# Kernel optimization log

Hardware: AMD Instinct MI355X
Metric: run time of the kernel (lower is better)

## Reference

```python
import jax, jax.numpy as jnp
import numpy as np

DIM = 256
NUM_HEADS = 4
HEAD_DIM = DIM // NUM_HEADS
SCALE = HEAD_DIM ** -0.5


def setup_inputs() -> dict:
    key = jax.random.key(0)
    ks = jax.random.split(key, 11)
    B, Nq, Nkv = 4, 2048, 2048
    inp = {
        "query_feat": jax.random.normal(ks[0], (B, Nq, DIM), dtype=jnp.float32),
        "key_value_feat": jax.random.normal(ks[1], (B, Nkv, DIM), dtype=jnp.float32),
        "reliability_kv": jax.random.uniform(ks[2], (B, Nkv), dtype=jnp.float32),
        "Wq": jax.random.normal(ks[3], (DIM, DIM), dtype=jnp.float32) * (DIM ** -0.5),
        "bq": jnp.zeros((DIM,), jnp.float32),
        "Wk": jax.random.normal(ks[4], (DIM, DIM), dtype=jnp.float32) * (DIM ** -0.5),
        "bk": jnp.zeros((DIM,), jnp.float32),
        "Wv": jax.random.normal(ks[5], (DIM, DIM), dtype=jnp.float32) * (DIM ** -0.5),
        "bv": jnp.zeros((DIM,), jnp.float32),
        "Wo": jax.random.normal(ks[6], (DIM, DIM), dtype=jnp.float32) * (DIM ** -0.5),
        "bo": jnp.zeros((DIM,), jnp.float32),
    }
    return inp


def _heads(x):
    B, N, C = x.shape
    return x.reshape(B, N, NUM_HEADS, HEAD_DIM).transpose(0, 2, 1, 3)  # [B,H,N,hd]


def reference(query_feat, key_value_feat, reliability_kv, Wq, bq, Wk, bk, Wv, bv, Wo, bo):
    B, Nq, _ = query_feat.shape
    q = _heads(query_feat @ Wq + bq)          # [B,H,Nq,hd]
    k = _heads(key_value_feat @ Wk + bk)      # [B,H,Nkv,hd]
    v = _heads(key_value_feat @ Wv + bv)
    # gate K/V by reliability (broadcast over heads and head_dim)
    rk = reliability_kv[:, None, :, None]     # [B,1,Nkv,1]
    k = k * rk
    v = v * rk
    attn = jnp.einsum("bhqd,bhkd->bhqk", q, k) * SCALE
    log_r = jnp.log(jnp.clip(reliability_kv, 1e-6))[:, None, None, :]  # [B,1,1,Nkv]
    attn = jax.nn.softmax(attn + log_r, axis=-1)  # [B,H,Nq,Nkv]
    out = jnp.einsum("bhqk,bhkd->bhqd", attn, v)
    out = out.transpose(0, 2, 1, 3).reshape(B, Nq, DIM)
    out = out @ Wo + bo
    attn_mean = attn.mean(axis=1)  # [B,Nq,Nkv]
    return out, attn_mean
```

## Files before the change

### kernel.cpp

```cpp
#include <hip/hip_runtime.h>


typedef __attribute__((ext_vector_type(8))) _Float16 half8;
typedef __attribute__((ext_vector_type(4))) _Float16 half4;
typedef __attribute__((ext_vector_type(2))) __fp16 fp16x2;
typedef __attribute__((ext_vector_type(4))) float f32x4;

#define MFMAH32(A, B, C) __builtin_amdgcn_mfma_f32_16x16x32_f16((A), (B), (C), 0, 0, 0)
#define MFMAH16(A, B, C) __builtin_amdgcn_mfma_f32_16x16x16f16((A), (B), (C), 0, 0, 0)

__device__ __forceinline__ unsigned short f2h(float f) {
    union { _Float16 h; unsigned short u; } c; c.h = (_Float16)f; return c.u;
}
__device__ __forceinline__ float h2f(unsigned short u) {
    union { unsigned short u; _Float16 h; } c; c.u = u; return (float)c.h;
}
__device__ __forceinline__ half8 ldh8(const unsigned short* p) {
    return *reinterpret_cast<const half8*>(p);
}
__device__ __forceinline__ half4 ldh4(const unsigned short* p) {
    return *reinterpret_cast<const half4*>(p);
}
__device__ __forceinline__ half4 pk4(float a, float b, float c, float d) {
    union { fp16x2 h2[2]; half4 h4; } u;
    u.h2[0] = __builtin_amdgcn_cvt_pkrtz(a, b);
    u.h2[1] = __builtin_amdgcn_cvt_pkrtz(c, d);
    return u.h4;
}
__device__ __forceinline__ void gld16(const unsigned short* g, unsigned short* l) {
    __builtin_amdgcn_global_load_lds(
        (const __attribute__((address_space(1))) unsigned int*)g,
        (__attribute__((address_space(3))) unsigned int*)l, 16, 0, 0);
}

__global__ void wsplit_kernel(const float* __restrict__ Wq, const float* __restrict__ Wk,
                              const float* __restrict__ Wv, const float* __restrict__ Wo,
                              unsigned short* __restrict__ WT) {
    int e = blockIdx.x * 256 + threadIdx.x;
    int m = e >> 16;
    int idx = e & 65535;
    int k = idx >> 8, n = idx & 255;
    const float* W = (m == 0) ? Wq : (m == 1) ? Wk : (m == 2) ? Wv : Wo;
    WT[m * 65536 + n * 256 + k] = f2h(W[idx]);
}

#define STAGE_W(dst_, src_, kt_) do {                                               \
    _Pragma("unroll")                                                               \
    for (int j_ = 0; j_ < 4; ++j_) {                                                \
        int s_ = w * 4 + j_;                                                        \
        int rowl_ = 8 * s_ + (l >> 3);                                              \
        int so_ = rowl_ * 256 + (kt_) * 64 + (((l & 7) ^ (rowl_ & 7)) << 3);        \
        gld16(&(src_)[so_], &(dst_)[s_ * 512]);                                     \
    }                                                                               \
} while (0)

#define GEMM_TILE(buf_, kt_) do {                                                   \
    _Pragma("unroll")                                                               \
    for (int ksl_ = 0; ksl_ < 2; ++ksl_) {                                          \
        _Pragma("unroll")                                                           \
        for (int n_ = 0; n_ < 16; ++n_) {                                           \
            int r_ = n_ * 16 + l15;                                                 \
            int idx_ = r_ * 64 + ((((ksl_)*4 + lg) ^ (r_ & 7)) << 3);               \
            half8 b_ = ldh8(&(buf_)[idx_]);                                         \
            acc[n_] = MFMAH32(ah[(kt_) * 2 + ksl_], b_, acc[n_]);                   \
        }                                                                           \
    }                                                                               \
} while (0)

__global__ __launch_bounds__(512, 1) void proj3_kernel(
    const float* __restrict__ query, const float* __restrict__ kv,
    const float* __restrict__ rel, const unsigned short* __restrict__ WT,
    const float* __restrict__ bq, const float* __restrict__ bk, const float* __restrict__ bv,
    unsigned short* __restrict__ Qh, unsigned short* __restrict__ Kh,
    unsigned short* __restrict__ Vtmp) {
    const int job = blockIdx.y;
    const float* X = (job == 0) ? query : kv;
    const unsigned short* wg = WT + job * 65536;
    const float* bias = (job == 0) ? bq : (job == 1) ? bk : bv;
    const float* rs = (job == 0) ? nullptr : rel;
    unsigned short* oh = (job == 0) ? Qh : (job == 1) ? Kh : Vtmp;

    __shared__ __align__(16) unsigned short wlds[2][256 * 64];

    const int w = threadIdx.x >> 6, l = threadIdx.x & 63;
    const int l15 = l & 15, lg = l >> 4;
    const int arow = blockIdx.x * 128 + w * 16 + l15;

    half8 ah[8];
#pragma unroll
    for (int ks = 0; ks < 8; ++ks) {
        const float* p = &X[arow * 256 + ks * 32 + lg * 8];
        float4 f0 = *reinterpret_cast<const float4*>(p);
        float4 f1 = *reinterpret_cast<const float4*>(p + 4);
        half8 t;
        t[0] = (_Float16)f0.x; t[1] = (_Float16)f0.y; t[2] = (_Float16)f0.z; t[3] = (_Float16)f0.w;
        t[4] = (_Float16)f1.x; t[5] = (_Float16)f1.y; t[6] = (_Float16)f1.z; t[7] = (_Float16)f1.w;
        ah[ks] = t;
    }
    f32x4 acc[16];
#pragma unroll
    for (int n = 0; n < 16; ++n) acc[n] = (f32x4){0.f, 0.f, 0.f, 0.f};

    STAGE_W(wlds[0], wg, 0);
    __syncthreads();
#pragma unroll
    for (int kt = 0; kt < 4; ++kt) {
        const int cur = kt & 1, nx = cur ^ 1;
        if (kt < 3) STAGE_W(wlds[nx], wg, kt + 1);
        GEMM_TILE(wlds[cur], kt);
        __syncthreads();
    }

    const int orow0 = blockIdx.x * 128 + w * 16 + lg * 4;
    float rsv[4];
#pragma unroll
    for (int r = 0; r < 4; ++r) rsv[r] = rs ? rs[orow0 + r] : 1.0f;
#pragma unroll
    for (int n = 0; n < 16; ++n) {
        const int col = n * 16 + l15;
        const float bn = bias[col];
#pragma unroll
        for (int r = 0; r < 4; ++r)
            oh[(orow0 + r) * 256 + col] = f2h((acc[n][r] + bn) * rsv[r]);
    }
}

__global__ void transpose_v_kernel(const unsigned short* __restrict__ Vtmp,
                                   unsigned short* __restrict__ Vt) {
    __shared__ unsigned short tile[16][264];
    const int st = blockIdx.x, b = blockIdx.y;
    const int t = threadIdx.x;
#pragma unroll
    for (int it = 0; it < 4; ++it) {
        int idx = it * 256 + t;
        int kr = idx >> 6;
        int d4 = (idx & 63) * 4;
        ushort4 v = *reinterpret_cast<const ushort4*>(
            &Vtmp[(size_t)(b * 2048 + st * 16 + kr) * 256 + d4]);
        tile[kr][d4 + 0] = v.x; tile[kr][d4 + 1] = v.y;
        tile[kr][d4 + 2] = v.z; tile[kr][d4 + 3] = v.w;
    }
    __syncthreads();
    {
        const int d = t;
        unsigned int u[8];
#pragma unroll
        for (int k2 = 0; k2 < 8; ++k2)
            u[k2] = (unsigned int)tile[k2 * 2][d] | ((unsigned int)tile[k2 * 2 + 1][d] << 16);
        uint4* dst = reinterpret_cast<uint4*>(&Vt[((size_t)(b * 128 + st) * 256 + d) * 16]);
        dst[0] = (uint4){u[0], u[1], u[2], u[3]};
        dst[1] = (uint4){u[4], u[5], u[6], u[7]};
    }
}

__global__ __launch_bounds__(256, 4) void attn_pass1(
    const unsigned short* __restrict__ Qh, const unsigned short* __restrict__ Kh,
    const unsigned short* __restrict__ Vt, const float* __restrict__ rel,
    float* __restrict__ po_a, float* __restrict__ po_b, float* __restrict__ ps) {
    const int bid = blockIdx.x;
    const int sw = (bid & 7) * 128 + (bid >> 3);
    const int b = sw >> 8;
    const int rem = sw & 255;
    const int kh = rem & 1;
    const int q0 = (rem >> 1) * 16;
    const int tid = threadIdx.x;
    const int w = tid >> 6, h = w;
    const int l = tid & 63, l15 = l & 15, lg = l >> 4;
    const float C2 = 0.18033688011112042f;

    __shared__ __align__(16) unsigned short ldsKV[2][4][2][1024];
    __shared__ float rel_lr[2048];

    {
        float4 v0 = reinterpret_cast<const float4*>(&rel[b * 2048])[tid * 2];
        float4 v1 = reinterpret_cast<const float4*>(&rel[b * 2048])[tid * 2 + 1];
        float* d = &rel_lr[tid * 8];
        d[0] = log2f(fmaxf(v0.x, 1e-6f)); d[1] = log2f(fmaxf(v0.y, 1e-6f));
        d[2] = log2f(fmaxf(v0.z, 1e-6f)); d[3] = log2f(fmaxf(v0.w, 1e-6f));
        d[4] = log2f(fmaxf(v1.x, 1e-6f)); d[5] = log2f(fmaxf(v1.y, 1e-6f));
        d[6] = log2f(fmaxf(v1.z, 1e-6f)); d[7] = log2f(fmaxf(v1.w, 1e-6f));
    }

    half8 qf0, qf1;
    {
        const int o0 = (b * 2048 + q0 + l15) * 256 + h * 64 + lg * 8;
        qf0 = ldh8(&Qh[o0]); qf1 = ldh8(&Qh[o0 + 32]);
    }
    __syncthreads();

    const int st0 = kh * 64;

    size_t kb_[2], vb_[2];
    {
        const int swzK = ((l & 7) ^ ((l >> 3) & 7)) << 3;
        const int swzV = ((l & 1) ^ ((l >> 1) & 1)) << 3;
#pragma unroll
        for (int j = 0; j < 2; ++j) {
            int kr = j * 8 + (l >> 3);
            kb_[j] = (size_t)(b * 2048 + st0 * 16 + kr) * 256 + h * 64 + swzK;
            int vd = j * 32 + (l >> 1);
            vb_[j] = (size_t)((b * 128 + st0) * 256 + h * 64 + vd) * 16 + swzV;
        }
    }
    unsigned short* myK = &ldsKV[0][w][0][0];
    unsigned short* myV = &ldsKV[1][w][0][0];
    const int kOff0 = l15 * 64 + ((lg ^ (l15 & 7)) << 3);
    const int kOff1 = l15 * 64 + (((4 + lg) ^ (l15 & 7)) << 3);
    int vOff[4];
#pragma unroll
    for (int dc = 0; dc < 4; ++dc)
        vOff[dc] = (dc * 16 + l15) * 16 + (((lg >> 1) ^ (l15 & 1)) << 3) + (lg & 1) * 4;

#define STG2(buf_, off_) do {                                                       \
    gld16(&Kh[kb_[0] + (off_)], &myK[(buf_) * 1024]);                               \
    gld16(&Kh[kb_[1] + (off_)], &myK[(buf_) * 1024 + 512]);                         \
    gld16(&Vt[vb_[0] + (off_)], &myV[(buf_) * 1024]);                               \
    gld16(&Vt[vb_[1] + (off_)], &myV[(buf_) * 1024 + 512]);                         \
} while (0)

    float ssum = 0.f;
    f32x4 oacc[4];
#pragma unroll
    for (int dc = 0; dc < 4; ++dc) oacc[dc] = (f32x4){0.f, 0.f, 0.f, 0.f};

    STG2(0, 0);
    size_t offn = 4096;
    for (int i = 0; i < 64; ++i) {
        const int cur = i & 1, nx = cur ^ 1;
        if (i < 63) {
            STG2(nx, offn); offn += 4096;
            asm volatile("s_waitcnt vmcnt(4)" ::: "memory");
        } else {
            asm volatile("s_waitcnt vmcnt(0)" ::: "memory");
        }
        __builtin_amdgcn_sched_barrier(0);
        half8 kf0 = ldh8(&myK[cur * 1024 + kOff0]);
        half8 kf1 = ldh8(&myK[cur * 1024 + kOff1]);
        f32x4 a = (f32x4){0.f, 0.f, 0.f, 0.f};
        a = MFMAH32(kf0, qf0, a);
        a = MFMAH32(kf1, qf1, a);
        float4 lr4 = *reinterpret_cast<const float4*>(&rel_lr[(st0 + i) * 16 + lg * 4]);
        float p0 = exp2f(__builtin_fmaf(a[0], C2, lr4.x));
        float p1 = exp2f(__builtin_fmaf(a[1], C2, lr4.y));
        float p2 = exp2f(__builtin_fmaf(a[2], C2, lr4.z));
        float p3 = exp2f(__builtin_fmaf(a[3], C2, lr4.w));
        ssum += (p0 + p1) + (p2 + p3);
        half4 pa = pk4(p0, p1, p2, p3);
#pragma unroll
        for (int dc = 0; dc < 4; ++dc) {
            half4 vf = ldh4(&myV[cur * 1024 + vOff[dc]]);
            oacc[dc] = MFMAH16(pa, vf, oacc[dc]);
        }
    }
#undef STG2

    float v = ssum;
    v += __shfl_xor(v, 16); v += __shfl_xor(v, 32);

    const int chunk = b * 2 + kh;
    float* po = (chunk < 2) ? (po_a + (size_t)chunk * 524288)
                            : (po_b + (size_t)(chunk - 2) * 524288);
#pragma unroll
    for (int dc = 0; dc < 4; ++dc)
#pragma unroll
        for (int r = 0; r < 4; ++r)
            po[(size_t)(q0 + lg * 4 + r) * 256 + h * 64 + dc * 16 + l15] = oacc[dc][r];
    if (l < 16)
        ps[(chunk * 4 + h) * 2048 + q0 + l] = v;
}

__global__ __launch_bounds__(256) void combine_kernel(
    const float* __restrict__ po_a, const float* __restrict__ po_b,
    const float* __restrict__ ps, unsigned short* __restrict__ AO,
    float* __restrict__ sinv_ws) {
    const int t = blockIdx.x * 256 + threadIdx.x;
    const int d4 = t & 63;
    const int bq = t >> 6;
    const int q = bq & 2047;
    const int b = bq >> 11;
    const int d0 = d4 * 4, h = d0 >> 6;
    const int c0 = b * 2, c1 = b * 2 + 1;
    const float* p0 = (c0 < 2) ? po_a + (size_t)c0 * 524288 : po_b + (size_t)(c0 - 2) * 524288;
    const float* p1 = (c1 < 2) ? po_a + (size_t)c1 * 524288 : po_b + (size_t)(c1 - 2) * 524288;
    float4 x = *reinterpret_cast<const float4*>(&p0[(size_t)q * 256 + d0]);
    float4 y = *reinterpret_cast<const float4*>(&p1[(size_t)q * 256 + d0]);
    float s = ps[(c0 * 4 + h) * 2048 + q] + ps[(c1 * 4 + h) * 2048 + q];
    float si = 1.0f / s;
    ushort4 o;
    o.x = f2h((x.x + y.x) * si); o.y = f2h((x.y + y.y) * si);
    o.z = f2h((x.z + y.z) * si); o.w = f2h((x.w + y.w) * si);
    *reinterpret_cast<ushort4*>(&AO[((size_t)(b * 2048 + q)) * 256 + d0]) = o;
    if (d4 == (h << 4)) sinv_ws[(b * 4 + h) * 2048 + q] = si;
}

__global__ __launch_bounds__(256, 4) void attn_mean_kernel(
    const unsigned short* __restrict__ Qh, const unsigned short* __restrict__ Kh,
    const float* __restrict__ rel, const float* __restrict__ sinv_ws,
    float* __restrict__ attn_mean) {
    const int kslice = blockIdx.x >> 7;
    const int inner = blockIdx.x & 127;
    const int sw = (inner & 7) * 16 + (inner >> 3);
    const int b = sw >> 5;
    const int q0 = (sw & 31) * 64;
    const int tid = threadIdx.x;
    const int w = tid >> 6;
    const int l = tid & 63, l15 = l & 15, lg = l >> 4;
    const int kb = b * 2048;
    const float C2 = 0.18033688011112042f;

    __shared__ __align__(16) unsigned short ldsK[2][8192];
    __shared__ float rel_lr[2048];

    {
        float4 v0 = reinterpret_cast<const float4*>(&rel[b * 2048])[tid * 2];
        float4 v1 = reinterpret_cast<const float4*>(&rel[b * 2048])[tid * 2 + 1];
        float* d = &rel_lr[tid * 8];
        d[0] = log2f(fmaxf(v0.x, 1e-6f)); d[1] = log2f(fmaxf(v0.y, 1e-6f));
        d[2] = log2f(fmaxf(v0.z, 1e-6f)); d[3] = log2f(fmaxf(v0.w, 1e-6f));
        d[4] = log2f(fmaxf(v1.x, 1e-6f)); d[5] = log2f(fmaxf(v1.y, 1e-6f));
        d[6] = log2f(fmaxf(v1.z, 1e-6f)); d[7] = log2f(fmaxf(v1.w, 1e-6f));
    }

    half8 qf[4][2];
    {
        const int qrow = b * 2048 + q0 + w * 16 + l15;
#pragma unroll
        for (int h = 0; h < 4; ++h)
#pragma unroll
            for (int kd = 0; kd < 2; ++kd)
                qf[h][kd] = ldh8(&Qh[qrow * 256 + h * 64 + kd * 32 + lg * 8]);
    }
    float lsi[4][4];
#pragma unroll
    for (int h = 0; h < 4; ++h)
#pragma unroll
        for (int r4 = 0; r4 < 4; ++r4)
            lsi[h][r4] = log2f(sinv_ws[(b * 4 + h) * 2048 + q0 + w * 16 + lg * 4 + r4]) - 2.0f;

    size_t kmb[4];
    {
#pragma unroll
        for (int j = 0; j < 4; ++j) {
            int s_ = w * 4 + j;
            int r_ = 2 * s_ + (l >> 5);
            kmb[j] = (size_t)(kb + r_) * 256 + (((l & 31) ^ (r_ & 7)) << 3);
        }
    }
#define STAGE_KM2(dst_, off_) do {                                                  \
    gld16(&Kh[kmb[0] + (off_)], &(dst_)[(w * 4 + 0) * 512]);                        \
    gld16(&Kh[kmb[1] + (off_)], &(dst_)[(w * 4 + 1) * 512]);                        \
    gld16(&Kh[kmb[2] + (off_)], &(dst_)[(w * 4 + 2) * 512]);                        \
    gld16(&Kh[kmb[3] + (off_)], &(dst_)[(w * 4 + 3) * 512]);                        \
} while (0)

    __syncthreads();

    const int kt0 = kslice * 8;
    size_t moff = (size_t)kt0 * 8192;
    STAGE_KM2(ldsK[0], moff);
    for (int ki = 0; ki < 8; ++ki) {
        const int kt = kt0 + ki;
        const int cur = ki & 1, nx = cur ^ 1;
        if (ki < 7) {
            STAGE_KM2(ldsK[nx], moff + 8192);
            moff += 8192;
            asm volatile("s_waitcnt vmcnt(4)" ::: "memory");
        } else {
            asm volatile("s_waitcnt vmcnt(0)" ::: "memory");
        }
        asm volatile("s_barrier" ::: "memory");
        __builtin_amdgcn_sched_barrier(0);
#pragma unroll
        for (int kc = 0; kc < 2; ++kc) {
            const int r = kc * 16 + l15;
            const int rx = r & 7;
            f32x4 a[4];
#pragma unroll
            for (int h = 0; h < 4; ++h) {
                half8 kf0 = ldh8(&ldsK[cur][r * 256 + (((h * 8 + lg) ^ rx) << 3)]);
                half8 kf1 = ldh8(&ldsK[cur][r * 256 + (((h * 8 + 4 + lg) ^ rx) << 3)]);
                f32x4 t = (f32x4){0.f, 0.f, 0.f, 0.f};
                t = MFMAH32(qf[h][0], kf0, t);
                t = MFMAH32(qf[h][1], kf1, t);
                a[h] = t;
            }
            const float lr = rel_lr[kt * 32 + kc * 16 + l15];
            const size_t kcol = (size_t)(kt * 32 + kc * 16 + l15);
#pragma unroll
            for (int r4 = 0; r4 < 4; ++r4) {
                float m = exp2f(__builtin_fmaf(a[0][r4], C2, lsi[0][r4]) + lr)
                        + exp2f(__builtin_fmaf(a[1][r4], C2, lsi[1][r4]) + lr)
                        + exp2f(__builtin_fmaf(a[2][r4], C2, lsi[2][r4]) + lr)
                        + exp2f(__builtin_fmaf(a[3][r4], C2, lsi[3][r4]) + lr);
                attn_mean[(size_t)(b * 2048 + q0 + w * 16 + lg * 4 + r4) * 2048 + kcol] = m;
            }
        }
        asm volatile("s_waitcnt lgkmcnt(0)\n\ts_barrier" ::: "memory");
    }
#undef STAGE_KM2
}

__global__ __launch_bounds__(512, 1) void final_kernel(
    const unsigned short* __restrict__ AO, const unsigned short* __restrict__ WoT,
    const float* __restrict__ bo, float* __restrict__ out) {
    __shared__ __align__(16) unsigned short wlds[2][256 * 64];

    const int w = threadIdx.x >> 6, l = threadIdx.x & 63;
    const int l15 = l & 15, lg = l >> 4;
    const int arow = blockIdx.x * 128 + w * 16 + l15;

    half8 ah[8];
#pragma unroll
    for (int ks = 0; ks < 8; ++ks)
        ah[ks] = ldh8(&AO[arow * 256 + ks * 32 + lg * 8]);
    f32x4 acc[16];
#pragma unroll
    for (int n = 0; n < 16; ++n) acc[n] = (f32x4){0.f, 0.f, 0.f, 0.f};

    STAGE_W(wlds[0], WoT, 0);
    __syncthreads();
#pragma unroll
    for (int kt = 0; kt < 4; ++kt) {
        const int cur = kt & 1, nx = cur ^ 1;
        if (kt < 3) STAGE_W(wlds[nx], WoT, kt + 1);
        GEMM_TILE(wlds[cur], kt);
        __syncthreads();
    }

    const int orow0 = blockIdx.x * 128 + w * 16 + lg * 4;
#pragma unroll
    for (int n = 0; n < 16; ++n) {
        const int col = n * 16 + l15;
        const float bn = bo[col];
#pragma unroll
        for (int r = 0; r < 4; ++r)
            out[(orow0 + r) * 256 + col] = acc[n][r] + bn;
    }
}

extern "C" void kernel_launch(void* const* d_in, const int* in_sizes, int n_in,
                              void* d_out, int out_size, void* d_ws, size_t ws_size,
                              hipStream_t stream) {
    const float* query = (const float*)d_in[0];
    const float* kv    = (const float*)d_in[1];
    const float* rel   = (const float*)d_in[2];
    const float* Wq    = (const float*)d_in[3];
    const float* bq    = (const float*)d_in[4];
    const float* Wk    = (const float*)d_in[5];
    const float* bk    = (const float*)d_in[6];
    const float* Wv    = (const float*)d_in[7];
    const float* bv    = (const float*)d_in[8];
    const float* Wo    = (const float*)d_in[9];
    const float* bo    = (const float*)d_in[10];

    char* ws = (char*)d_ws;
    unsigned short* WT   = (unsigned short*)(ws + 0);
    unsigned short* Qh   = (unsigned short*)(ws + 524288);
    unsigned short* Kh   = (unsigned short*)(ws + 4718592);
    unsigned short* Vtmp = (unsigned short*)(ws + 8912896);
    unsigned short* Vt   = (unsigned short*)(ws + 13107200);
    unsigned short* AO   = (unsigned short*)(ws + 17301504);
    float*          sinv = (float*)(ws + 21495808);
    float*          ps   = (float*)(ws + 21626880);
    float*          po_b = (float*)(ws + 21889024);
    float*          po_a = (float*)Vtmp;

    float* out = (float*)d_out;
    float* attn_mean = (float*)d_out + 2097152;

    wsplit_kernel<<<1024, 256, 0, stream>>>(Wq, Wk, Wv, Wo, WT);
    proj3_kernel<<<dim3(64, 3), 512, 0, stream>>>(query, kv, rel, WT,
                                                  bq, bk, bv, Qh, Kh, Vtmp);
    transpose_v_kernel<<<dim3(128, 4), 256, 0, stream>>>(Vtmp, Vt);
    attn_pass1<<<1024, 256, 0, stream>>>(Qh, Kh, Vt, rel, po_a, po_b, ps);
    combine_kernel<<<2048, 256, 0, stream>>>(po_a, po_b, ps, AO, sinv);
    attn_mean_kernel<<<1024, 256, 0, stream>>>(Qh, Kh, rel, sinv, attn_mean);
    final_kernel<<<64, 512, 0, stream>>>(AO, WT + 3 * 65536, bo, out);
}
```

Before: 115.9 us.

## Process two query tiles per wave and split KV range across wave pairs in attention pass

Each block now covers 32 queries with 512 threads. Each wave computes two 16-query tiles against the same K tile, so every K and V fragment is reused twice. The KV range is split between two wave groups whose partial outputs and sums are reduced through LDS before being written. V fragments are now loaded directly from global memory into registers instead of staged in LDS, which halves the LDS traffic per step. The cost is more registers, an LDS reduction step with extra syncs, and fewer blocks (512 instead of 1024), which may lower occupancy and load balance.

```diff
diff --git a/kernel.cpp b/kernel.cpp
--- a/kernel.cpp
+++ b/kernel.cpp
@@ -153,120 +153,170 @@
     }
 }
 
-__global__ __launch_bounds__(256, 4) void attn_pass1(
+__global__ __launch_bounds__(512, 4) void attn_pass1(
     const unsigned short* __restrict__ Qh, const unsigned short* __restrict__ Kh,
     const unsigned short* __restrict__ Vt, const float* __restrict__ rel,
     float* __restrict__ po_a, float* __restrict__ po_b, float* __restrict__ ps) {
     const int bid = blockIdx.x;
-    const int sw = (bid & 7) * 128 + (bid >> 3);
-    const int b = sw >> 8;
-    const int rem = sw & 255;
+    const int sw = (bid & 7) * 64 + (bid >> 3);
+    const int b = sw >> 7;
+    const int rem = sw & 127;
     const int kh = rem & 1;
-    const int q0 = (rem >> 1) * 16;
+    const int q0 = (rem >> 1) * 32;
     const int tid = threadIdx.x;
-    const int w = tid >> 6, h = w;
+    const int w = tid >> 6, h = w & 3, ks = w >> 2;
     const int l = tid & 63, l15 = l & 15, lg = l >> 4;
     const float C2 = 0.18033688011112042f;
 
-    __shared__ __align__(16) unsigned short ldsKV[2][4][2][1024];
+    __shared__ __align__(16) unsigned short ldsK[8][2][1024];
     __shared__ float rel_lr[2048];
+    __shared__ float ssum_sh[2][4][2][16];
 
     {
-        float4 v0 = reinterpret_cast<const float4*>(&rel[b * 2048])[tid * 2];
-        float4 v1 = reinterpret_cast<const float4*>(&rel[b * 2048])[tid * 2 + 1];
-        float* d = &rel_lr[tid * 8];
-        d[0] = log2f(fmaxf(v0.x, 1e-6f)); d[1] = log2f(fmaxf(v0.y, 1e-6f));
-        d[2] = log2f(fmaxf(v0.z, 1e-6f)); d[3] = log2f(fmaxf(v0.w, 1e-6f));
-        d[4] = log2f(fmaxf(v1.x, 1e-6f)); d[5] = log2f(fmaxf(v1.y, 1e-6f));
-        d[6] = log2f(fmaxf(v1.z, 1e-6f)); d[7] = log2f(fmaxf(v1.w, 1e-6f));
-    }
-
-    half8 qf0, qf1;
-    {
-        const int o0 = (b * 2048 + q0 + l15) * 256 + h * 64 + lg * 8;
-        qf0 = ldh8(&Qh[o0]); qf1 = ldh8(&Qh[o0 + 32]);
-    }
-    __syncthreads();
-
-    const int st0 = kh * 64;
-
-    size_t kb_[2], vb_[2];
+        float4 v = reinterpret_cast<const float4*>(&rel[b * 2048])[tid];
+        float* d = &rel_lr[tid * 4];
+        d[0] = log2f(fmaxf(v.x, 1e-6f)); d[1] = log2f(fmaxf(v.y, 1e-6f));
+        d[2] = log2f(fmaxf(v.z, 1e-6f)); d[3] = log2f(fmaxf(v.w, 1e-6f));
+    }
+
+    half8 qf[2][2];
+#pragma unroll
+    for (int qs = 0; qs < 2; ++qs)
+#pragma unroll
+        for (int kd = 0; kd < 2; ++kd)
+            qf[qs][kd] = ldh8(&Qh[(b * 2048 + q0 + qs * 16 + l15) * 256 +
+                                  h * 64 + kd * 32 + lg * 8]);
+    __syncthreads();
+
+    const int st0 = kh * 64 + ks * 32;
+
+    size_t kb_[2];
     {
         const int swzK = ((l & 7) ^ ((l >> 3) & 7)) << 3;
-        const int swzV = ((l & 1) ^ ((l >> 1) & 1)) << 3;
 #pragma unroll
         for (int j = 0; j < 2; ++j) {
             int kr = j * 8 + (l >> 3);
             kb_[j] = (size_t)(b * 2048 + st0 * 16 + kr) * 256 + h * 64 + swzK;
-            int vd = j * 32 + (l >> 1);
-            vb_[j] = (size_t)((b * 128 + st0) * 256 + h * 64 + vd) * 16 + swzV;
         }
     }
-    unsigned short* myK = &ldsKV[0][w][0][0];
-    unsigned short* myV = &ldsKV[1][w][0][0];
+    size_t va_[4];
+#pragma unroll
+    for (int dc = 0; dc < 4; ++dc)
+        va_[dc] = ((size_t)((b * 128 + st0) * 256) + h * 64 + dc * 16 + l15) * 16 + lg * 4;
+
+    unsigned short* myK = &ldsK[w][0][0];
     const int kOff0 = l15 * 64 + ((lg ^ (l15 & 7)) << 3);
     const int kOff1 = l15 * 64 + (((4 + lg) ^ (l15 & 7)) << 3);
-    int vOff[4];
-#pragma unroll
-    for (int dc = 0; dc < 4; ++dc)
-        vOff[dc] = (dc * 16 + l15) * 16 + (((lg >> 1) ^ (l15 & 1)) << 3) + (lg & 1) * 4;
-
-#define STG2(buf_, off_) do {                                                       \
-    gld16(&Kh[kb_[0] + (off_)], &myK[(buf_) * 1024]);                               \
-    gld16(&Kh[kb_[1] + (off_)], &myK[(buf_) * 1024 + 512]);                         \
-    gld16(&Vt[vb_[0] + (off_)], &myV[(buf_) * 1024]);                               \
-    gld16(&Vt[vb_[1] + (off_)], &myV[(buf_) * 1024 + 512]);                         \
+
+#define STGK(buf_, i_) do {                                                         \
+    gld16(&Kh[kb_[0] + (size_t)(i_) * 4096], &myK[(buf_) * 1024]);                  \
+    gld16(&Kh[kb_[1] + (size_t)(i_) * 4096], &myK[(buf_) * 1024 + 512]);            \
 } while (0)
-
-    float ssum = 0.f;
-    f32x4 oacc[4];
-#pragma unroll
-    for (int dc = 0; dc < 4; ++dc) oacc[dc] = (f32x4){0.f, 0.f, 0.f, 0.f};
-
-    STG2(0, 0);
-    size_t offn = 4096;
-    for (int i = 0; i < 64; ++i) {
-        const int cur = i & 1, nx = cur ^ 1;
-        if (i < 63) {
-            STG2(nx, offn); offn += 4096;
-            asm volatile("s_waitcnt vmcnt(4)" ::: "memory");
-        } else {
-            asm volatile("s_waitcnt vmcnt(0)" ::: "memory");
+#define VLOADM(dst_, i_) do {                                                       \
+    dst_[0] = ldh4(&Vt[va_[0] + (size_t)(i_) * 4096]);                              \
+    dst_[1] = ldh4(&Vt[va_[1] + (size_t)(i_) * 4096]);                              \
+    dst_[2] = ldh4(&Vt[va_[2] + (size_t)(i_) * 4096]);                              \
+    dst_[3] = ldh4(&Vt[va_[3] + (size_t)(i_) * 4096]);                              \
+} while (0)
+
+    float ssum0 = 0.f, ssum1 = 0.f;
+    f32x4 oacc0[4], oacc1[4];
+#pragma unroll
+    for (int dc = 0; dc < 4; ++dc) {
+        oacc0[dc] = (f32x4){0.f, 0.f, 0.f, 0.f};
+        oacc1[dc] = (f32x4){0.f, 0.f, 0.f, 0.f};
+    }
+
+#define COMPUTE(step_, BUF_, VF_) do {                                              \
+    half8 kf0 = ldh8(&myK[(BUF_) * 1024 + kOff0]);                                  \
+    half8 kf1 = ldh8(&myK[(BUF_) * 1024 + kOff1]);                                  \
+    f32x4 a0 = (f32x4){0.f, 0.f, 0.f, 0.f}, a1 = a0;                                \
+    a0 = MFMAH32(kf0, qf[0][0], a0); a0 = MFMAH32(kf1, qf[0][1], a0);               \
+    a1 = MFMAH32(kf0, qf[1][0], a1); a1 = MFMAH32(kf1, qf[1][1], a1);               \
+    float4 lr4 = *reinterpret_cast<const float4*>(                                  \
+        &rel_lr[(st0 + (step_)) * 16 + lg * 4]);                                    \
+    float p00 = exp2f(__builtin_fmaf(a0[0], C2, lr4.x));                            \
+    float p01 = exp2f(__builtin_fmaf(a0[1], C2, lr4.y));                            \
+    float p02 = exp2f(__builtin_fmaf(a0[2], C2, lr4.z));                            \
+    float p03 = exp2f(__builtin_fmaf(a0[3], C2, lr4.w));                            \
+    float p10 = exp2f(__builtin_fmaf(a1[0], C2, lr4.x));                            \
+    float p11 = exp2f(__builtin_fmaf(a1[1], C2, lr4.y));                            \
+    float p12 = exp2f(__builtin_fmaf(a1[2], C2, lr4.z));                            \
+    float p13 = exp2f(__builtin_fmaf(a1[3], C2, lr4.w));                            \
+    ssum0 += (p00 + p01) + (p02 + p03);                                             \
+    ssum1 += (p10 + p11) + (p12 + p13);                                             \
+    half4 pa0 = pk4(p00, p01, p02, p03);                                            \
+    half4 pa1 = pk4(p10, p11, p12, p13);                                            \
+    _Pragma("unroll")                                                               \
+    for (int dc = 0; dc < 4; ++dc) {                                                \
+        oacc0[dc] = MFMAH16(pa0, VF_[dc], oacc0[dc]);                               \
+        oacc1[dc] = MFMAH16(pa1, VF_[dc], oacc1[dc]);                               \
+    }                                                                               \
+} while (0)
+
+    half4 vfa[4], vfb[4];
+    STGK(0, 0);
+    VLOADM(vfa, 0);
+    for (int i = 0; i < 32; i += 2) {
+        STGK(1, i + 1);
+        VLOADM(vfb, i + 1);
+        asm volatile("s_waitcnt vmcnt(6)" ::: "memory");
+        __builtin_amdgcn_sched_barrier(0);
+        COMPUTE(i, 0, vfa);
+        {
+            const int nxt = (i + 2 < 32) ? i + 2 : 31;
+            STGK(0, nxt);
+            VLOADM(vfa, nxt);
         }
+        asm volatile("s_waitcnt vmcnt(6)" ::: "memory");
         __builtin_amdgcn_sched_barrier(0);
-        half8 kf0 = ldh8(&myK[cur * 1024 + kOff0]);
-        half8 kf1 = ldh8(&myK[cur * 1024 + kOff1]);
-        f32x4 a = (f32x4){0.f, 0.f, 0.f, 0.f};
-        a = MFMAH32(kf0, qf0, a);
-        a = MFMAH32(kf1, qf1, a);
-        float4 lr4 = *reinterpret_cast<const float4*>(&rel_lr[(st0 + i) * 16 + lg * 4]);
-        float p0 = exp2f(__builtin_fmaf(a[0], C2, lr4.x));
-        float p1 = exp2f(__builtin_fmaf(a[1], C2, lr4.y));
-        float p2 = exp2f(__builtin_fmaf(a[2], C2, lr4.z));
-        float p3 = exp2f(__builtin_fmaf(a[3], C2, lr4.w));
-        ssum += (p0 + p1) + (p2 + p3);
-        half4 pa = pk4(p0, p1, p2, p3);
-#pragma unroll
-        for (int dc = 0; dc < 4; ++dc) {
-            half4 vf = ldh4(&myV[cur * 1024 + vOff[dc]]);
-            oacc[dc] = MFMAH16(pa, vf, oacc[dc]);
+        COMPUTE(i + 1, 1, vfb);
+    }
+    asm volatile("s_waitcnt vmcnt(0)" ::: "memory");
+#undef STGK
+#undef VLOADM
+#undef COMPUTE
+
+    float vr0 = ssum0, vr1 = ssum1;
+    vr0 += __shfl_xor(vr0, 16); vr0 += __shfl_xor(vr0, 32);
+    vr1 += __shfl_xor(vr1, 16); vr1 += __shfl_xor(vr1, 32);
+
+    __syncthreads();
+    if (l < 16) { ssum_sh[ks][h][0][l] = vr0; ssum_sh[ks][h][1][l] = vr1; }
+    float* obuf = (float*)&ldsK[0][0][0];
+    if (ks == 1) {
+#pragma unroll
+        for (int qs = 0; qs < 2; ++qs)
+#pragma unroll
+            for (int dc = 0; dc < 4; ++dc)
+#pragma unroll
+                for (int r = 0; r < 4; ++r)
+                    obuf[(qs * 16 + lg * 4 + r) * 256 + h * 64 + dc * 16 + l15] =
+                        (qs == 0) ? oacc0[dc][r] : oacc1[dc][r];
+    }
+    __syncthreads();
+    if (ks == 0) {
+        const int chunk = b * 2 + kh;
+        float* po = (chunk < 2) ? (po_a + (size_t)chunk * 524288)
+                                : (po_b + (size_t)(chunk - 2) * 524288);
+#pragma unroll
+        for (int qs = 0; qs < 2; ++qs)
+#pragma unroll
+            for (int dc = 0; dc < 4; ++dc)
+#pragma unroll
+                for (int r = 0; r < 4; ++r) {
+                    const int d = h * 64 + dc * 16 + l15;
+                    const int q = qs * 16 + lg * 4 + r;
+                    const float mine = (qs == 0) ? oacc0[dc][r] : oacc1[dc][r];
+                    po[(size_t)(q0 + q) * 256 + d] = mine + obuf[q * 256 + d];
+                }
+        if (l < 16) {
+            ps[(chunk * 4 + h) * 2048 + q0 + l] =
+                ssum_sh[0][h][0][l] + ssum_sh[1][h][0][l];
+            ps[(chunk * 4 + h) * 2048 + q0 + 16 + l] =
+                ssum_sh[0][h][1][l] + ssum_sh[1][h][1][l];
         }
     }
-#undef STG2
-
-    float v = ssum;
-    v += __shfl_xor(v, 16); v += __shfl_xor(v, 32);
-
-    const int chunk = b * 2 + kh;
-    float* po = (chunk < 2) ? (po_a + (size_t)chunk * 524288)
-                            : (po_b + (size_t)(chunk - 2) * 524288);
-#pragma unroll
-    for (int dc = 0; dc < 4; ++dc)
-#pragma unroll
-        for (int r = 0; r < 4; ++r)
-            po[(size_t)(q0 + lg * 4 + r) * 256 + h * 64 + dc * 16 + l15] = oacc[dc][r];
-    if (l < 16)
-        ps[(chunk * 4 + h) * 2048 + q0 + l] = v;
 }
 
 __global__ __launch_bounds__(256) void combine_kernel(
@@ -472,7 +522,7 @@
     proj3_kernel<<<dim3(64, 3), 512, 0, stream>>>(query, kv, rel, WT,
                                                   bq, bk, bv, Qh, Kh, Vtmp);
     transpose_v_kernel<<<dim3(128, 4), 256, 0, stream>>>(Vtmp, Vt);
-    attn_pass1<<<1024, 256, 0, stream>>>(Qh, Kh, Vt, rel, po_a, po_b, ps);
+    attn_pass1<<<512, 512, 0, stream>>>(Qh, Kh, Vt, rel, po_a, po_b, ps);
     combine_kernel<<<2048, 256, 0, stream>>>(po_a, po_b, ps, AO, sinv);
     attn_mean_kernel<<<1024, 256, 0, stream>>>(Qh, Kh, rel, sinv, attn_mean);
     final_kernel<<<64, 512, 0, stream>>>(AO, WT + 3 * 65536, bo, out);
```

Result: faster. 105.0 us (-9.4%).
